# Kernel tuning notes

Measured on AMD Instinct MI355X. Metric: run time of the kernel, lower is better.

Reference implementation:

```python
import jax, jax.numpy as jnp
import numpy as np

N_NODES = 50000
N_EDGES = 800000
IN_DIM = 128
HID = 256


def _gcn_conv(x, src, dst, norm, W, b, n_nodes):
    # PyG GCNConv: h = x @ W; out[dst] += norm * h[src]; out += b
    h = x @ W                                   # [N, out_dim]
    msgs = h[src] * norm[:, None]               # [E+N, out_dim]
    agg = jax.ops.segment_sum(msgs, dst, num_segments=n_nodes)
    return agg + b


def _gcn_norm(src, dst, n_nodes):
    # add self-loops and compute symmetric normalization deg^-1/2 A_hat deg^-1/2
    loops = jnp.arange(n_nodes, dtype=src.dtype)
    src2 = jnp.concatenate([src, loops])
    dst2 = jnp.concatenate([dst, loops])
    deg = jax.ops.segment_sum(jnp.ones_like(dst2, dtype=jnp.float32), dst2,
                              num_segments=n_nodes)
    dis = jnp.where(deg > 0, jax.lax.rsqrt(deg), 0.0)
    norm = dis[src2] * dis[dst2]
    return src2, dst2, norm


def setup_inputs() -> dict:
    key = jax.random.key(0)
    ks = jax.random.split(key, 5)
    x = jax.random.normal(ks[0], (N_NODES, IN_DIM), dtype=jnp.float32)
    edge_index = jax.random.randint(ks[1], (2, N_EDGES), 0, N_NODES, dtype=jnp.int64)
    W1 = jax.random.normal(ks[2], (IN_DIM, HID), dtype=jnp.float32) / np.sqrt(IN_DIM)
    b1 = jnp.zeros((HID,), dtype=jnp.float32)
    W2 = jax.random.normal(ks[3], (HID, HID // 2), dtype=jnp.float32) / np.sqrt(HID)
    b2 = jnp.zeros((HID // 2,), dtype=jnp.float32)
    Wfc = jax.random.normal(ks[4], (HID // 2, 1), dtype=jnp.float32) / np.sqrt(HID // 2)
    bfc = jnp.zeros((1,), dtype=jnp.float32)
    return {"x": x, "edge_index": edge_index, "W1": W1, "b1": b1,
            "W2": W2, "b2": b2, "Wfc": Wfc, "bfc": bfc}


def reference(x, edge_index, W1, b1, W2, b2, Wfc, bfc):
    n_nodes = x.shape[0]
    src, dst = edge_index[0], edge_index[1]
    src2, dst2, norm = _gcn_norm(src, dst, n_nodes)
    h = jax.nn.relu(_gcn_conv(x, src2, dst2, norm, W1, b1, n_nodes))
    h = jax.nn.relu(_gcn_conv(h, src2, dst2, norm, W2, b2, n_nodes))
    pooled = h.mean(axis=0)                     # [HID//2]
    return pooled @ Wfc + bfc                   # [1]
```

## Files before the change

### kernel.cpp

```cpp
#include <hip/hip_runtime.h>
#include <hip/hip_bf16.h>

#define N_NODES 50000
#define N_EDGES 800000
#define IN_DIM  128
#define HID     256
#define HID2    128
#define BUCKET  64

using bf16x8 = __attribute__((ext_vector_type(8))) short;
using f32x4  = __attribute__((ext_vector_type(4))) float;

static __device__ __forceinline__ unsigned f2bf(float f) {
    unsigned u = __float_as_uint(f);
    return (u + 0x7FFFu + ((u >> 16) & 1u)) >> 16;
}
static __device__ __forceinline__ float bflo(unsigned u) { return __uint_as_float(u << 16); }
static __device__ __forceinline__ float bfhi(unsigned u) { return __uint_as_float(u & 0xFFFF0000u); }

__global__ void fill_bucket(const int* __restrict__ ei, int* __restrict__ cur,
                            int* __restrict__ srcs) {
    int e = blockIdx.x * blockDim.x + threadIdx.x;
    if (e < N_EDGES) {
        int d = ei[N_EDGES + e];
        int o = atomicAdd(&cur[d], 1);
        if (o < BUCKET) srcs[(d << 6) + o] = ei[e];
    }
}

__global__ __launch_bounds__(256)
void pack_wts(const float* __restrict__ W1, const float* __restrict__ W2,
              unsigned short* __restrict__ WT1, unsigned short* __restrict__ WT2,
              float* __restrict__ accbuf) {
    int t = blockIdx.x * 256 + threadIdx.x;
    if (t == 0) accbuf[0] = 0.f;
    if (t < IN_DIM * HID) {
        int n = t / IN_DIM, k = t - n * IN_DIM;
        WT1[t] = (unsigned short)f2bf(W1[(size_t)k * HID + n]);
    } else {
        int t2 = t - IN_DIM * HID;
        int n = t2 / HID, k = t2 - n * HID;
        WT2[t2] = (unsigned short)f2bf(W2[(size_t)k * HID2 + n]);
    }
}

__global__ __launch_bounds__(256)
void pack_x_scaled(const float* __restrict__ in, const int* __restrict__ deg,
                   unsigned* __restrict__ out) {
    int t = blockIdx.x * 256 + threadIdx.x;
    float d = rsqrtf((float)(deg[t >> 5] + 1));
    float4 v = ((const float4*)in)[t];
    uint2 p;
    p.x = f2bf(d * v.x) | (f2bf(d * v.y) << 16);
    p.y = f2bf(d * v.z) | (f2bf(d * v.w) << 16);
    ((uint2*)out)[t] = p;
}

__global__ __launch_bounds__(256)
void agg_x_bf16(const unsigned* __restrict__ Xb, const int* __restrict__ deg,
                const int* __restrict__ srcs, unsigned* __restrict__ Ab) {
    int wid = threadIdx.x >> 6, lane = threadIdx.x & 63;
    int i = blockIdx.x * 4 + wid;
    unsigned sv = Xb[(size_t)i * 64 + lane];
    float a0 = bflo(sv), a1 = bfhi(sv);
    int dg = deg[i];
    int e = i << 6, e1 = e + min(dg, BUCKET);
    for (; e + 3 < e1; e += 4) {
        int s0 = srcs[e], s1 = srcs[e + 1], s2 = srcs[e + 2], s3 = srcs[e + 3];
        unsigned v0 = Xb[(size_t)s0 * 64 + lane];
        unsigned v1 = Xb[(size_t)s1 * 64 + lane];
        unsigned v2 = Xb[(size_t)s2 * 64 + lane];
        unsigned v3 = Xb[(size_t)s3 * 64 + lane];
        a0 += (bflo(v0) + bflo(v1)) + (bflo(v2) + bflo(v3));
        a1 += (bfhi(v0) + bfhi(v1)) + (bfhi(v2) + bfhi(v3));
    }
    for (; e < e1; ++e) {
        unsigned v = Xb[(size_t)srcs[e] * 64 + lane];
        a0 += bflo(v); a1 += bfhi(v);
    }
    float di = rsqrtf((float)(dg + 1));
    Ab[(size_t)i * 64 + lane] = f2bf(di * a0) | (f2bf(di * a1) << 16);
}

__global__ __launch_bounds__(256)
void agg_g_pool_bf16(const unsigned* __restrict__ Gb, const int* __restrict__ deg,
                     const int* __restrict__ srcs, const float* __restrict__ b2,
                     const float* __restrict__ wfc, float* __restrict__ pernode) {
    int wid = threadIdx.x >> 6, lane = threadIdx.x & 63;
    int i = blockIdx.x * 4 + wid;
    unsigned sv = Gb[(size_t)i * 64 + lane];
    float a0 = bflo(sv), a1 = bfhi(sv);
    int dg = deg[i];
    int e = i << 6, e1 = e + min(dg, BUCKET);
    for (; e + 3 < e1; e += 4) {
        int s0 = srcs[e], s1 = srcs[e + 1], s2 = srcs[e + 2], s3 = srcs[e + 3];
        unsigned v0 = Gb[(size_t)s0 * 64 + lane];
        unsigned v1 = Gb[(size_t)s1 * 64 + lane];
        unsigned v2 = Gb[(size_t)s2 * 64 + lane];
        unsigned v3 = Gb[(size_t)s3 * 64 + lane];
        a0 += (bflo(v0) + bflo(v1)) + (bflo(v2) + bflo(v3));
        a1 += (bfhi(v0) + bfhi(v1)) + (bfhi(v2) + bfhi(v3));
    }
    for (; e < e1; ++e) {
        unsigned v = Gb[(size_t)srcs[e] * 64 + lane];
        a0 += bflo(v); a1 += bfhi(v);
    }
    float di = rsqrtf((float)(dg + 1));
    int c0 = lane * 2;
    float r = fmaxf(di * a0 + b2[c0], 0.f) * wfc[c0]
            + fmaxf(di * a1 + b2[c0 + 1], 0.f) * wfc[c0 + 1];
#pragma unroll
    for (int off = 32; off > 0; off >>= 1) r += __shfl_down(r, off, 64);
    if (lane == 0) pernode[i] = r;
}

__global__ __launch_bounds__(256)
void reduce_pernode(const float* __restrict__ pn, float* __restrict__ accbuf) {
    __shared__ float red[256];
    float s = 0.f;
    for (int i = blockIdx.x * 256 + threadIdx.x; i < N_NODES; i += gridDim.x * 256)
        s += pn[i];
    red[threadIdx.x] = s;
    __syncthreads();
    for (int off = 128; off > 0; off >>= 1) {
        if (threadIdx.x < off) red[threadIdx.x] += red[threadIdx.x + off];
        __syncthreads();
    }
    if (threadIdx.x == 0) atomicAdd(accbuf, red[0]);
}

__global__ void finalize(const float* __restrict__ accbuf,
                         const float* __restrict__ bfc, float* __restrict__ out) {
    out[0] = accbuf[0] * (1.0f / (float)N_NODES) + bfc[0];
}

template<int MODE>
__global__ __launch_bounds__(256)
void gemm_mfma(const unsigned short* __restrict__ A,
               const unsigned short* __restrict__ WT,
               const float* __restrict__ bias,
               const int* __restrict__ deg,
               unsigned short* __restrict__ C,
               int M, int N, int K) {
    __shared__ __align__(16) unsigned short Asl[4 * 64 * 8];
    __shared__ __align__(16) unsigned short Bsl[4 * 128 * 8];

    int tid = threadIdx.x;
    int lane = tid & 63, w = tid >> 6;
    int wr = w >> 1, wc = w & 1;
    int row0 = blockIdx.x * 64;
    int col0 = blockIdx.y * 128;

    f32x4 acc[2][4];
#pragma unroll
    for (int i = 0; i < 2; ++i)
#pragma unroll
        for (int j = 0; j < 4; ++j) acc[i][j] = (f32x4){0.f, 0.f, 0.f, 0.f};

    int arow = min(row0 + (tid & 63), M - 1);
    const unsigned short* agp = A + (size_t)arow * K + (tid >> 6) * 8;
    const unsigned short* bgp0 = WT + (size_t)(col0 + (tid & 127)) * K + (tid >> 7) * 8;
    const unsigned short* bgp1 = bgp0 + 16;

    const bf16x8* Av = (const bf16x8*)Asl;
    const bf16x8* Bv = (const bf16x8*)Bsl;
    int aidx = (lane >> 4) * 64 + wr * 32 + (lane & 15);
    int bidx = (lane >> 4) * 128 + wc * 64 + (lane & 15);

    for (int k0 = 0; k0 < K; k0 += 32) {
        *(float4*)&Asl[tid * 8]         = *(const float4*)(agp + k0);
        *(float4*)&Bsl[tid * 8]         = *(const float4*)(bgp0 + k0);
        *(float4*)&Bsl[(tid + 256) * 8] = *(const float4*)(bgp1 + k0);
        __syncthreads();

        bf16x8 af[2], bf[4];
#pragma unroll
        for (int fm = 0; fm < 2; ++fm) af[fm] = Av[aidx + fm * 16];
#pragma unroll
        for (int fn = 0; fn < 4; ++fn) bf[fn] = Bv[bidx + fn * 16];
#pragma unroll
        for (int fm = 0; fm < 2; ++fm)
#pragma unroll
            for (int fn = 0; fn < 4; ++fn)
                acc[fm][fn] = __builtin_amdgcn_mfma_f32_16x16x32_bf16(
                    af[fm], bf[fn], acc[fm][fn], 0, 0, 0);
        __syncthreads();
    }

    float bv[4];
    if (MODE == 0) {
#pragma unroll
        for (int fn = 0; fn < 4; ++fn)
            bv[fn] = bias[col0 + wc * 64 + fn * 16 + (lane & 15)];
    }
#pragma unroll
    for (int fm = 0; fm < 2; ++fm) {
#pragma unroll
        for (int r = 0; r < 4; ++r) {
            int row = row0 + wr * 32 + fm * 16 + (lane >> 4) * 4 + r;
            if (row < M) {
                float rsc = (MODE == 1) ? rsqrtf((float)(deg[row] + 1)) : 0.f;
#pragma unroll
                for (int fn = 0; fn < 4; ++fn) {
                    int col = col0 + wc * 64 + fn * 16 + (lane & 15);
                    float v = acc[fm][fn][r];
                    if (MODE == 0) v = fmaxf(v + bv[fn], 0.f);
                    else           v = v * rsc;
                    C[(size_t)row * N + col] = (unsigned short)f2bf(v);
                }
            }
        }
    }
}

extern "C" void kernel_launch(void* const* d_in, const int* in_sizes, int n_in,
                              void* d_out, int out_size, void* d_ws, size_t ws_size,
                              hipStream_t stream) {
    const float* x   = (const float*)d_in[0];
    const int*   ei  = (const int*)d_in[1];
    const float* W1  = (const float*)d_in[2];
    const float* b1  = (const float*)d_in[3];
    const float* W2  = (const float*)d_in[4];
    const float* b2  = (const float*)d_in[5];
    const float* Wfc = (const float*)d_in[6];
    const float* bfc = (const float*)d_in[7];
    float* out = (float*)d_out;

    char* ws = (char*)d_ws;
    size_t off = 0;
    auto carve = [&](size_t bytes) {
        void* p = ws + off;
        off += (bytes + 255) & ~(size_t)255;
        return p;
    };
    int*   cur   = (int*)carve((size_t)N_NODES * 4);
    int*   srcs  = (int*)carve((size_t)N_NODES * BUCKET * 4);
    unsigned* Xb = (unsigned*)carve((size_t)N_NODES * 64 * 4);
    unsigned* Ab = (unsigned*)carve((size_t)N_NODES * 64 * 4);
    unsigned short* h1b = (unsigned short*)carve((size_t)N_NODES * HID * 2);
    unsigned short* Gb  = (unsigned short*)carve((size_t)N_NODES * HID2 * 2);
    unsigned short* WT1 = (unsigned short*)carve((size_t)HID * IN_DIM * 2);
    unsigned short* WT2 = (unsigned short*)carve((size_t)HID2 * HID * 2);
    float* pernode = (float*)carve((size_t)N_NODES * 4);
    float* accbuf  = (float*)carve(4);

    hipMemsetAsync(cur, 0, (size_t)N_NODES * 4, stream);

    const int TB = 256;
    const int EB = (N_EDGES + TB - 1) / TB;

    pack_wts<<<(IN_DIM * HID + HID * HID2) / TB, TB, 0, stream>>>(W1, W2, WT1, WT2, accbuf);

    fill_bucket<<<EB, TB, 0, stream>>>(ei, cur, srcs);

    pack_x_scaled<<<(N_NODES * IN_DIM / 4) / TB, TB, 0, stream>>>(x, cur, Xb);

    agg_x_bf16<<<N_NODES / 4, TB, 0, stream>>>(Xb, cur, srcs, Ab);
    {
        dim3 grid((N_NODES + 63) / 64, HID / 128);
        gemm_mfma<0><<<grid, TB, 0, stream>>>((const unsigned short*)Ab, WT1, b1,
                                              nullptr, h1b, N_NODES, HID, IN_DIM);
    }
    {
        dim3 grid((N_NODES + 63) / 64, HID2 / 128);
        gemm_mfma<1><<<grid, TB, 0, stream>>>(h1b, WT2, nullptr, cur,
                                              Gb, N_NODES, HID2, HID);
    }
    agg_g_pool_bf16<<<N_NODES / 4, TB, 0, stream>>>((const unsigned*)Gb, cur, srcs,
                                                    b2, Wfc, pernode);
    reduce_pernode<<<32, TB, 0, stream>>>(pernode, accbuf);
    finalize<<<1, 1, 0, stream>>>(accbuf, bfc, out);
}
```

Before: 191.1 us.

## Sort bucket sources per wave, merge reduce/finalize, fold memset into weight pack

Each aggregation wave loads its whole source bucket into lanes, sorts it with a 64-lane bitonic network, and broadcasts indices by shuffle, with an 8-way unrolled gather. The aim is better gather locality and fewer index loads. The hipMemset of the degree counters is folded into the weight-packing kernel, fill_bucket handles two edges per thread, and the two-stage pooled reduction plus finalize becomes one single-block kernel. The bitonic sort adds about 21 shuffle steps per node, and the ordering of launches is relied on for zeroing cur before fill_bucket.

```diff
diff --git a/kernel.cpp b/kernel.cpp
--- a/kernel.cpp
+++ b/kernel.cpp
@@ -3,6 +3,7 @@
 
 #define N_NODES 50000
 #define N_EDGES 800000
+#define EHALF   400000
 #define IN_DIM  128
 #define HID     256
 #define HID2    128
@@ -18,22 +19,42 @@
 static __device__ __forceinline__ float bflo(unsigned u) { return __uint_as_float(u << 16); }
 static __device__ __forceinline__ float bfhi(unsigned u) { return __uint_as_float(u & 0xFFFF0000u); }
 
+static __device__ __forceinline__ int bucket_sort64(int v, int lane) {
+#pragma unroll
+    for (int k = 2; k <= 64; k <<= 1) {
+#pragma unroll
+        for (int j = k >> 1; j > 0; j >>= 1) {
+            int p = __shfl_xor(v, j, 64);
+            int mn = min(v, p), mx = max(v, p);
+            bool up = ((lane & k) == 0);
+            bool lower = ((lane & j) == 0);
+            v = (up == lower) ? mn : mx;
+        }
+    }
+    return v;
+}
+
 __global__ void fill_bucket(const int* __restrict__ ei, int* __restrict__ cur,
                             int* __restrict__ srcs) {
     int e = blockIdx.x * blockDim.x + threadIdx.x;
-    if (e < N_EDGES) {
-        int d = ei[N_EDGES + e];
-        int o = atomicAdd(&cur[d], 1);
-        if (o < BUCKET) srcs[(d << 6) + o] = ei[e];
+    if (e < EHALF) {
+        int s0 = ei[e];
+        int s1 = ei[EHALF + e];
+        int d0 = ei[N_EDGES + e];
+        int d1 = ei[N_EDGES + EHALF + e];
+        int o0 = atomicAdd(&cur[d0], 1);
+        int o1 = atomicAdd(&cur[d1], 1);
+        if (o0 < BUCKET) srcs[(d0 << 6) + o0] = s0;
+        if (o1 < BUCKET) srcs[(d1 << 6) + o1] = s1;
     }
 }
 
 __global__ __launch_bounds__(256)
 void pack_wts(const float* __restrict__ W1, const float* __restrict__ W2,
               unsigned short* __restrict__ WT1, unsigned short* __restrict__ WT2,
-              float* __restrict__ accbuf) {
+              int* __restrict__ cur) {
     int t = blockIdx.x * 256 + threadIdx.x;
-    if (t == 0) accbuf[0] = 0.f;
+    if (t < N_NODES) cur[t] = 0;
     if (t < IN_DIM * HID) {
         int n = t / IN_DIM, k = t - n * IN_DIM;
         WT1[t] = (unsigned short)f2bf(W1[(size_t)k * HID + n]);
@@ -63,22 +84,30 @@
     int i = blockIdx.x * 4 + wid;
     unsigned sv = Xb[(size_t)i * 64 + lane];
     float a0 = bflo(sv), a1 = bfhi(sv);
-    int dg = deg[i];
-    int e = i << 6, e1 = e + min(dg, BUCKET);
-    for (; e + 3 < e1; e += 4) {
-        int s0 = srcs[e], s1 = srcs[e + 1], s2 = srcs[e + 2], s3 = srcs[e + 3];
-        unsigned v0 = Xb[(size_t)s0 * 64 + lane];
-        unsigned v1 = Xb[(size_t)s1 * 64 + lane];
-        unsigned v2 = Xb[(size_t)s2 * 64 + lane];
-        unsigned v3 = Xb[(size_t)s3 * 64 + lane];
-        a0 += (bflo(v0) + bflo(v1)) + (bflo(v2) + bflo(v3));
-        a1 += (bfhi(v0) + bfhi(v1)) + (bfhi(v2) + bfhi(v3));
-    }
-    for (; e < e1; ++e) {
-        unsigned v = Xb[(size_t)srcs[e] * 64 + lane];
+    int dgr = deg[i];
+    int dg = min(dgr, BUCKET);
+    int se = (lane < dg) ? srcs[(i << 6) + lane] : 0x7FFFFFFF;
+    se = bucket_sort64(se, lane);
+    int j = 0;
+    for (; j + 8 <= dg; j += 8) {
+        unsigned v0 = Xb[(size_t)__shfl(se, j + 0, 64) * 64 + lane];
+        unsigned v1 = Xb[(size_t)__shfl(se, j + 1, 64) * 64 + lane];
+        unsigned v2 = Xb[(size_t)__shfl(se, j + 2, 64) * 64 + lane];
+        unsigned v3 = Xb[(size_t)__shfl(se, j + 3, 64) * 64 + lane];
+        unsigned v4 = Xb[(size_t)__shfl(se, j + 4, 64) * 64 + lane];
+        unsigned v5 = Xb[(size_t)__shfl(se, j + 5, 64) * 64 + lane];
+        unsigned v6 = Xb[(size_t)__shfl(se, j + 6, 64) * 64 + lane];
+        unsigned v7 = Xb[(size_t)__shfl(se, j + 7, 64) * 64 + lane];
+        a0 += ((bflo(v0) + bflo(v1)) + (bflo(v2) + bflo(v3)))
+            + ((bflo(v4) + bflo(v5)) + (bflo(v6) + bflo(v7)));
+        a1 += ((bfhi(v0) + bfhi(v1)) + (bfhi(v2) + bfhi(v3)))
+            + ((bfhi(v4) + bfhi(v5)) + (bfhi(v6) + bfhi(v7)));
+    }
+    for (; j < dg; ++j) {
+        unsigned v = Xb[(size_t)__shfl(se, j, 64) * 64 + lane];
         a0 += bflo(v); a1 += bfhi(v);
     }
-    float di = rsqrtf((float)(dg + 1));
+    float di = rsqrtf((float)(dgr + 1));
     Ab[(size_t)i * 64 + lane] = f2bf(di * a0) | (f2bf(di * a1) << 16);
 }
 
@@ -90,22 +119,30 @@
     int i = blockIdx.x * 4 + wid;
     unsigned sv = Gb[(size_t)i * 64 + lane];
     float a0 = bflo(sv), a1 = bfhi(sv);
-    int dg = deg[i];
-    int e = i << 6, e1 = e + min(dg, BUCKET);
-    for (; e + 3 < e1; e += 4) {
-        int s0 = srcs[e], s1 = srcs[e + 1], s2 = srcs[e + 2], s3 = srcs[e + 3];
-        unsigned v0 = Gb[(size_t)s0 * 64 + lane];
-        unsigned v1 = Gb[(size_t)s1 * 64 + lane];
-        unsigned v2 = Gb[(size_t)s2 * 64 + lane];
-        unsigned v3 = Gb[(size_t)s3 * 64 + lane];
-        a0 += (bflo(v0) + bflo(v1)) + (bflo(v2) + bflo(v3));
-        a1 += (bfhi(v0) + bfhi(v1)) + (bfhi(v2) + bfhi(v3));
-    }
-    for (; e < e1; ++e) {
-        unsigned v = Gb[(size_t)srcs[e] * 64 + lane];
+    int dgr = deg[i];
+    int dg = min(dgr, BUCKET);
+    int se = (lane < dg) ? srcs[(i << 6) + lane] : 0x7FFFFFFF;
+    se = bucket_sort64(se, lane);
+    int j = 0;
+    for (; j + 8 <= dg; j += 8) {
+        unsigned v0 = Gb[(size_t)__shfl(se, j + 0, 64) * 64 + lane];
+        unsigned v1 = Gb[(size_t)__shfl(se, j + 1, 64) * 64 + lane];
+        unsigned v2 = Gb[(size_t)__shfl(se, j + 2, 64) * 64 + lane];
+        unsigned v3 = Gb[(size_t)__shfl(se, j + 3, 64) * 64 + lane];
+        unsigned v4 = Gb[(size_t)__shfl(se, j + 4, 64) * 64 + lane];
+        unsigned v5 = Gb[(size_t)__shfl(se, j + 5, 64) * 64 + lane];
+        unsigned v6 = Gb[(size_t)__shfl(se, j + 6, 64) * 64 + lane];
+        unsigned v7 = Gb[(size_t)__shfl(se, j + 7, 64) * 64 + lane];
+        a0 += ((bflo(v0) + bflo(v1)) + (bflo(v2) + bflo(v3)))
+            + ((bflo(v4) + bflo(v5)) + (bflo(v6) + bflo(v7)));
+        a1 += ((bfhi(v0) + bfhi(v1)) + (bfhi(v2) + bfhi(v3)))
+            + ((bfhi(v4) + bfhi(v5)) + (bfhi(v6) + bfhi(v7)));
+    }
+    for (; j < dg; ++j) {
+        unsigned v = Gb[(size_t)__shfl(se, j, 64) * 64 + lane];
         a0 += bflo(v); a1 += bfhi(v);
     }
-    float di = rsqrtf((float)(dg + 1));
+    float di = rsqrtf((float)(dgr + 1));
     int c0 = lane * 2;
     float r = fmaxf(di * a0 + b2[c0], 0.f) * wfc[c0]
             + fmaxf(di * a1 + b2[c0 + 1], 0.f) * wfc[c0 + 1];
@@ -114,24 +151,25 @@
     if (lane == 0) pernode[i] = r;
 }
 
-__global__ __launch_bounds__(256)
-void reduce_pernode(const float* __restrict__ pn, float* __restrict__ accbuf) {
-    __shared__ float red[256];
-    float s = 0.f;
-    for (int i = blockIdx.x * 256 + threadIdx.x; i < N_NODES; i += gridDim.x * 256)
-        s += pn[i];
-    red[threadIdx.x] = s;
+__global__ __launch_bounds__(1024)
+void reduce_final(const float* __restrict__ pn, const float* __restrict__ bfc,
+                  float* __restrict__ out) {
+    __shared__ float red[1024];
+    int tid = threadIdx.x;
+    float s0 = 0.f, s1 = 0.f, s2 = 0.f, s3 = 0.f;
+    for (int i = tid; i < N_NODES; i += 4096) {
+        s0 += pn[i];
+        if (i + 1024 < N_NODES) s1 += pn[i + 1024];
+        if (i + 2048 < N_NODES) s2 += pn[i + 2048];
+        if (i + 3072 < N_NODES) s3 += pn[i + 3072];
+    }
+    red[tid] = (s0 + s1) + (s2 + s3);
     __syncthreads();
-    for (int off = 128; off > 0; off >>= 1) {
-        if (threadIdx.x < off) red[threadIdx.x] += red[threadIdx.x + off];
+    for (int off = 512; off > 0; off >>= 1) {
+        if (tid < off) red[tid] += red[tid + off];
         __syncthreads();
     }
-    if (threadIdx.x == 0) atomicAdd(accbuf, red[0]);
-}
-
-__global__ void finalize(const float* __restrict__ accbuf,
-                         const float* __restrict__ bfc, float* __restrict__ out) {
-    out[0] = accbuf[0] * (1.0f / (float)N_NODES) + bfc[0];
+    if (tid == 0) out[0] = red[0] * (1.0f / (float)N_NODES) + bfc[0];
 }
 
 template<int MODE>
@@ -242,16 +280,12 @@
     unsigned short* WT1 = (unsigned short*)carve((size_t)HID * IN_DIM * 2);
     unsigned short* WT2 = (unsigned short*)carve((size_t)HID2 * HID * 2);
     float* pernode = (float*)carve((size_t)N_NODES * 4);
-    float* accbuf  = (float*)carve(4);
-
-    hipMemsetAsync(cur, 0, (size_t)N_NODES * 4, stream);
 
     const int TB = 256;
-    const int EB = (N_EDGES + TB - 1) / TB;
-
-    pack_wts<<<(IN_DIM * HID + HID * HID2) / TB, TB, 0, stream>>>(W1, W2, WT1, WT2, accbuf);
-
-    fill_bucket<<<EB, TB, 0, stream>>>(ei, cur, srcs);
+
+    pack_wts<<<(IN_DIM * HID + HID * HID2) / TB, TB, 0, stream>>>(W1, W2, WT1, WT2, cur);
+
+    fill_bucket<<<(EHALF + TB - 1) / TB, TB, 0, stream>>>(ei, cur, srcs);
 
     pack_x_scaled<<<(N_NODES * IN_DIM / 4) / TB, TB, 0, stream>>>(x, cur, Xb);
 
@@ -268,6 +302,5 @@
     }
     agg_g_pool_bf16<<<N_NODES / 4, TB, 0, stream>>>((const unsigned*)Gb, cur, srcs,
                                                     b2, Wfc, pernode);
-    reduce_pernode<<<32, TB, 0, stream>>>(pernode, accbuf);
-    finalize<<<1, 1, 0, stream>>>(accbuf, bfc, out);
-}
+    reduce_final<<<1, 1024, 0, stream>>>(pernode, bfc, out);
+}
```

Result: no change. 189.3 us (-1.0%).
